# Kernel tuning notes

Measured on AMD Instinct MI355X. Metric: run time of the kernel, lower is better.

The kernel has to match this reference:

```python
import jax, jax.numpy as jnp
import numpy as np

N_NODES = 50000
N_EDGES = 800000
HID = 64
N_LAYERS = 3
N_GRAPHS = 64
NEG_SLOPE = 0.01  # nn.LeakyReLU default


def setup_inputs() -> dict:
    key = jax.random.key(0)
    ks = jax.random.split(key, 10)
    return {
        "x": jax.random.normal(ks[0], (N_NODES, HID), dtype=jnp.float32),
        "edge_attr": jax.random.normal(ks[1], (N_EDGES,), dtype=jnp.float32),
        "edge_w": jax.random.normal(ks[2], (N_LAYERS, 1, HID), dtype=jnp.float32) * 0.1,
        "edge_b": jax.random.normal(ks[3], (N_LAYERS, HID), dtype=jnp.float32) * 0.1,
        "node_w": jax.random.normal(ks[4], (N_LAYERS, 2 * HID, HID), dtype=jnp.float32) * 0.05,
        "node_b": jax.random.normal(ks[5], (N_LAYERS, HID), dtype=jnp.float32) * 0.1,
        "fc_w": jax.random.normal(ks[6], (HID, 1), dtype=jnp.float32) * 0.1,
        "fc_b": jax.random.normal(ks[7], (1,), dtype=jnp.float32) * 0.1,
        "edge_index": jax.random.randint(ks[8], (2, N_EDGES), 0, N_NODES, dtype=jnp.int32),
        "batch": jnp.sort(jax.random.randint(ks[9], (N_NODES,), 0, N_GRAPHS, dtype=jnp.int32)),
    }


def reference(x, edge_attr, edge_w, edge_b, node_w, node_b, fc_w, fc_b, edge_index, batch):
    src = edge_index[0]  # x_j gathered from source nodes
    dst = edge_index[1]  # aggregated into target nodes (aggr='add')
    ea = edge_attr.reshape(-1, 1)  # [E, 1]
    for l in range(N_LAYERS):
        edge_emb = ea @ edge_w[l] + edge_b[l]                       # [E, H] edge MLP
        msg = jnp.concatenate([x[src], edge_emb], axis=1)            # [E, 2H] message
        aggr = jax.ops.segment_sum(msg, dst, num_segments=N_NODES)   # [N, 2H] scatter-add
        x = jax.nn.relu(aggr @ node_w[l] + node_b[l])                # update: node MLP + ReLU
        x = jnp.where(x >= 0, x, NEG_SLOPE * x)                      # LeakyReLU (dropout=0)
    # global_mean_pool over batch assignment
    sums = jax.ops.segment_sum(x, batch, num_segments=N_GRAPHS)      # [G, H]
    counts = jax.ops.segment_sum(jnp.ones((x.shape[0], 1), x.dtype), batch, num_segments=N_GRAPHS)
    pooled = sums / jnp.maximum(counts, 1.0)
    return pooled @ fc_w + fc_b  # [G, 1]
```

## Files before the change

### kernel.cpp

```cpp
#include <hip/hip_runtime.h>

#define N_NODES 50000
#define N_EDGES 800000
#define HID 64
#define N_LAYERS 3
#define N_GRAPHS 64
#define MAXDEG 64
#define FIXS 4096.0f
#define NBUCK 196
#define CAP 8064
#define SCB 4096

typedef unsigned int u32;
typedef unsigned short ushort_t;
typedef short bf16x8 __attribute__((ext_vector_type(8)));
typedef float f32x4 __attribute__((ext_vector_type(4)));
typedef float f32x2 __attribute__((ext_vector_type(2)));

__device__ __forceinline__ ushort_t f2bf(float f) {
    unsigned int u = __builtin_bit_cast(unsigned int, f);
    unsigned int r = u + 0x7fffu + ((u >> 16) & 1u);
    return (ushort_t)(r >> 16);
}
__device__ __forceinline__ unsigned char f2fp8(float f) {
    u32 p = __builtin_amdgcn_cvt_pk_fp8_f32(f, f, 0u, false);
    return (unsigned char)(p & 0xFFu);
}

__global__ __launch_bounds__(256) void cvt_gb_uv_kernel(
        const float* __restrict__ x_in, uint2* __restrict__ xf8,
        const int* __restrict__ batch, int* __restrict__ gstart,
        int* __restrict__ bucketCur,
        const float* __restrict__ edge_w, const float* __restrict__ edge_b,
        const float* __restrict__ node_w, float* __restrict__ uv,
        const float* __restrict__ fc_b, float* __restrict__ out,
        int cvtBlocks, int gbBlocks) {
    int t = threadIdx.x;
    int b = (int)blockIdx.x;
    if (b < cvtBlocks) {
        int i = b * 256 + t;
        if (i < N_NODES * HID / 8) {
            const float4* p = (const float4*)(x_in + (size_t)i * 8);
            float4 a = p[0], c = p[1];
            u32 lo = __builtin_amdgcn_cvt_pk_fp8_f32(a.x, a.y, 0u, false);
            lo      = __builtin_amdgcn_cvt_pk_fp8_f32(a.z, a.w, lo, true);
            u32 hi = __builtin_amdgcn_cvt_pk_fp8_f32(c.x, c.y, 0u, false);
            hi      = __builtin_amdgcn_cvt_pk_fp8_f32(c.z, c.w, hi, true);
            uint2 o; o.x = lo; o.y = hi;
            xf8[i] = o;
        }
        return;
    }
    if (b < cvtBlocks + gbBlocks) {
        int i = (b - cvtBlocks) * 256 + t;
        if (i >= N_NODES) return;
        if (i < NBUCK) bucketCur[i] = i * CAP;
        int bi = batch[i];
        if (i == 0) {
            for (int g = 0; g <= bi; g++) gstart[g] = 0;
        } else {
            int bp = batch[i - 1];
            for (int g = bp + 1; g <= bi; g++) gstart[g] = i;
        }
        if (i == N_NODES - 1) {
            for (int g = bi + 1; g <= N_GRAPHS; g++) gstart[g] = N_NODES;
        }
        return;
    }
    if (t >= 192) {
        if (t < 192 + N_GRAPHS) out[t - 192] = fc_b[0];
        return;
    }
    int l = t >> 6, hp = t & 63;
    const float* w2 = node_w + l * 2 * HID * HID + HID * HID + hp;
    float u = 0.f, v = 0.f;
    for (int h = 0; h < HID; h++) {
        float w = w2[h * HID];
        u += edge_w[l * HID + h] * w;
        v += edge_b[l * HID + h] * w;
    }
    uv[l * 2 * HID + hp]       = u;
    uv[l * 2 * HID + HID + hp] = v;
}

__global__ __launch_bounds__(256) void scatter_kernel(
        const int* __restrict__ src, const int* __restrict__ dst,
        const float* __restrict__ ea, int* __restrict__ bucketCur,
        uint2* __restrict__ recs) {
    __shared__ u32 hist[256], pfx[256], excl[256], baseL[256], limL[256];
    __shared__ uint2 stage[SCB];
    int t = threadIdx.x;
    int b0 = blockIdx.x * SCB;
    int nE = N_EDGES - b0; if (nE > SCB) nE = SCB;
    hist[t] = 0;
    __syncthreads();
    for (int i = t; i < nE; i += 256)
        atomicAdd(&hist[(dst[b0 + i] >> 8) & 255], 1u);
    __syncthreads();
    pfx[t] = hist[t];
    __syncthreads();
    for (int off = 1; off < 256; off <<= 1) {
        u32 v = (t >= off) ? pfx[t - off] : 0u;
        __syncthreads();
        pfx[t] += v;
        __syncthreads();
    }
    u32 cntv = hist[t];
    u32 ex = pfx[t] - cntv;
    excl[t] = ex;
    u32 gbase = (u32)t * CAP;
    if (cntv > 0 && t < NBUCK) {
        gbase = (u32)atomicAdd(&bucketCur[t], (int)cntv);
        u32 lim = (u32)(t + 1) * CAP;
        if (gbase + cntv > lim) cntv = (gbase < lim) ? (lim - gbase) : 0u;
    }
    baseL[t] = gbase;
    limL[t]  = ex + cntv;
    hist[t]  = ex;
    __syncthreads();
    for (int i = t; i < nE; i += 256) {
        int e = b0 + i;
        int d = dst[e];
        int s = src[e];
        float fv = (ea[e] + 8.0f) * FIXS;
        fv = fminf(fmaxf(fv, 0.0f), 65535.0f);
        u32 fx = __float2uint_rn(fv);
        u32 idx = atomicAdd(&hist[(d >> 8) & 255], 1u);
        uint2 r; r.x = (u32)s | (fx << 16); r.y = (u32)d;
        if (idx < (u32)SCB) stage[idx] = r;
    }
    __syncthreads();
    for (int i = t; i < nE; i += 256) {
        uint2 r = stage[i];
        u32 bk = (r.y >> 8) & 255;
        if (bk < NBUCK && (u32)i < limL[bk])
            recs[(size_t)baseL[bk] + ((u32)i - excl[bk])] = r;
    }
}

__global__ __launch_bounds__(256) void build_ell_kernel(
        const uint2* __restrict__ recs, const int* __restrict__ bucketCur,
        u32* __restrict__ ell, int* __restrict__ cnt) {
    __shared__ u32 hist[256], pfx[256], excl[256];
    __shared__ u32 stagePay[CAP];
    __shared__ ushort_t nodeOf[CAP];
    int t = threadIdx.x;
    int b = blockIdx.x;
    size_t eBase = (size_t)b * CAP;
    int m = bucketCur[b] - b * CAP;
    if (m > CAP) m = CAP;
    if (m < 0) m = 0;
    hist[t] = 0;
    __syncthreads();
    for (int i = t; i < m; i += 256)
        atomicAdd(&hist[recs[eBase + i].y & 255], 1u);
    __syncthreads();
    pfx[t] = hist[t];
    __syncthreads();
    for (int off = 1; off < 256; off <<= 1) {
        u32 v = (t >= off) ? pfx[t - off] : 0u;
        __syncthreads();
        pfx[t] += v;
        __syncthreads();
    }
    u32 full = hist[t];
    u32 ex = pfx[t] - full;
    excl[t] = ex;
    u32 cv = full > MAXDEG ? MAXDEG : full;
    int node = b * 256 + t;
    if (node < N_NODES) cnt[node] = (int)cv;
    for (u32 r = 0; r < full && (ex + r) < (u32)CAP; r++) nodeOf[ex + r] = (ushort_t)t;
    hist[t] = ex;
    __syncthreads();
    for (int i = t; i < m; i += 256) {
        uint2 r = recs[eBase + i];
        u32 idx = atomicAdd(&hist[r.y & 255], 1u);
        if (idx < (u32)CAP) stagePay[idx] = r.x;
    }
    __syncthreads();
    for (int i = t; i < m; i += 256) {
        u32 n8 = nodeOf[i];
        u32 rank = (u32)i - excl[n8];
        if (rank < MAXDEG)
            ell[((size_t)(b * 256 + n8) << 6) + rank] = stagePay[i];
    }
}

__global__ __launch_bounds__(256) void agg_mfma_kernel(
        const unsigned char* __restrict__ xf8, const u32* __restrict__ ell,
        const int* __restrict__ cnt,
        const float* __restrict__ W1, const float* __restrict__ node_b_l,
        const float* __restrict__ uv_l, float* __restrict__ sattr,
        int layer0, unsigned char* __restrict__ out_f8, float* __restrict__ out_f32) {
    __shared__ float red[4][64][9];
    __shared__ u32   redS[4][8];
    int lane = threadIdx.x & 63;
    int w = threadIdx.x >> 6;
    int nodeBase = blockIdx.x * 16;
    int oct = lane & 7, n8 = lane >> 3;
    int pairSel = w >> 1;
    int kslice = w & 1;

    int m = nodeBase + pairSel * 8 + n8;
    int dg = cnt[m]; if (dg > MAXDEG) dg = MAXDEG;
    int mx = dg;
#pragma unroll
    for (int off = 8; off < 64; off <<= 1) {
        int o = __shfl_xor(mx, off);
        mx = o > mx ? o : mx;
    }

    const uint4* erow4 = (const uint4*)(ell + ((size_t)m << 6));
    const uint2* xrows = (const uint2*)xf8;
    float accC[8] = {0,0,0,0,0,0,0,0};
    u32 sfix = 0;
    int base = kslice * 4;
    uint4 e4 = {0, 0, 0, 0};
    if (base < mx) e4 = erow4[base >> 2];
    for (; base < mx; base += 8) {
        int nbase = base + 8;
        uint4 e4n = {0, 0, 0, 0};
        if (nbase < mx) e4n = erow4[nbase >> 2];
        u32 ee[4] = {e4.x, e4.y, e4.z, e4.w};
        uint2 rw[4];
        float f[4];
#pragma unroll
        for (int k = 0; k < 4; k++) {
            bool v = (base + k) < dg;
            sfix += (v && oct == 0) ? (ee[k] >> 16) : 0u;
            int s = v ? (int)(ee[k] & 0xffffu) : 0;
            rw[k] = xrows[(size_t)s * 8 + oct];
            f[k] = v ? 1.0f : 0.0f;
        }
#pragma unroll
        for (int k = 0; k < 4; k++) {
            f32x2 p0 = __builtin_amdgcn_cvt_pk_f32_fp8(rw[k].x, false);
            f32x2 p1 = __builtin_amdgcn_cvt_pk_f32_fp8(rw[k].x, true);
            f32x2 p2 = __builtin_amdgcn_cvt_pk_f32_fp8(rw[k].y, false);
            f32x2 p3 = __builtin_amdgcn_cvt_pk_f32_fp8(rw[k].y, true);
            accC[0] += f[k] * p0[0]; accC[1] += f[k] * p0[1];
            accC[2] += f[k] * p1[0]; accC[3] += f[k] * p1[1];
            accC[4] += f[k] * p2[0]; accC[5] += f[k] * p2[1];
            accC[6] += f[k] * p3[0]; accC[7] += f[k] * p3[1];
        }
        e4 = e4n;
    }

#pragma unroll
    for (int j = 0; j < 8; j++) red[w][lane][j] = accC[j];
    if (oct == 0) redS[w][n8] = sfix;
    __syncthreads();
    if (w != 0) return;

    int q = lane >> 4, n15 = lane & 15;
    int w0 = (n15 >> 3) * 2;
    int h8 = (n15 & 7) * 8;
    float accA[8], accB[8];
#pragma unroll
    for (int j = 0; j < 8; j++) {
        accA[j] = red[w0][h8 + q][j]     + red[w0 + 1][h8 + q][j];
        accB[j] = red[w0][h8 + 4 + q][j] + red[w0 + 1][h8 + 4 + q][j];
    }
    u32 sfix2 = redS[w0][n15 & 7] + redS[w0 + 1][n15 & 7];
    int m2 = nodeBase + n15;
    int dg2 = cnt[m2]; if (dg2 > MAXDEG) dg2 = MAXDEG;

    float satv;
    if (layer0) {
        satv = (float)(int)sfix2 * (1.0f / FIXS) - 8.0f * (float)dg2;
        if (lane < 16) sattr[m2] = satv;
    } else {
        satv = sattr[m2];
    }

    bf16x8 af0, af1;
#pragma unroll
    for (int j = 0; j < 8; j++) {
        af0[j] = (short)f2bf(accA[j]);
        af1[j] = (short)f2bf(accB[j]);
    }

    int q8 = q * 8;
    f32x4 c[4];
#pragma unroll
    for (int nt = 0; nt < 4; nt++) {
        bf16x8 b0, b1;
#pragma unroll
        for (int j = 0; j < 8; j++) {
            b0[j] = (short)f2bf(W1[(q8 + j) * HID + nt * 16 + n15]);
            b1[j] = (short)f2bf(W1[(32 + q8 + j) * HID + nt * 16 + n15]);
        }
        f32x4 z = {0.f, 0.f, 0.f, 0.f};
        c[nt] = __builtin_amdgcn_mfma_f32_16x16x32_bf16(af0, b0, z, 0, 0, 0);
        c[nt] = __builtin_amdgcn_mfma_f32_16x16x32_bf16(af1, b1, c[nt], 0, 0, 0);
    }

    float dgown = (float)dg2;
    float sat[4], dgf[4];
#pragma unroll
    for (int r = 0; r < 4; r++) {
        int srcLane = q * 4 + r;
        sat[r] = __shfl(satv, srcLane);
        dgf[r] = __shfl(dgown, srcLane);
    }
#pragma unroll
    for (int nt = 0; nt < 4; nt++) {
        int col = nt * 16 + n15;
        float uc = uv_l[col], vc = uv_l[HID + col], bc = node_b_l[col];
#pragma unroll
        for (int r = 0; r < 4; r++) {
            int n = nodeBase + q * 4 + r;
            float val = c[nt][r] + sat[r] * uc + dgf[r] * vc + bc;
            val = val > 0.f ? val : 0.f;
            if (out_f8) out_f8[(size_t)n * HID + col] = f2fp8(val);
            else        out_f32[(size_t)n * HID + col] = val;
        }
    }
}

__global__ __launch_bounds__(256) void pool_fc_kernel(
        const float* __restrict__ x, const int* __restrict__ gstart,
        const float* __restrict__ fc_w, float* __restrict__ out) {
    __shared__ float red[4][HID];
    int g = blockIdx.x >> 3, s8 = blockIdx.x & 7;
    int lane = threadIdx.x & 63, w = threadIdx.x >> 6;
    int s = gstart[g], e = gstart[g + 1];
    float acc = 0.f;
    int r = s + s8 * 4 + w;
    for (; r + 96 < e; r += 128) {
        float a0 = x[(size_t)(r     ) * HID + lane];
        float a1 = x[(size_t)(r + 32) * HID + lane];
        float a2 = x[(size_t)(r + 64) * HID + lane];
        float a3 = x[(size_t)(r + 96) * HID + lane];
        acc += a0 + a1 + a2 + a3;
    }
    for (; r < e; r += 32) acc += x[(size_t)r * HID + lane];
    red[w][lane] = acc;
    __syncthreads();
    if (w != 0) return;
    acc = red[0][lane] + red[1][lane] + red[2][lane] + red[3][lane];
    float dot = acc * fc_w[lane];
    for (int off = 32; off > 0; off >>= 1) dot += __shfl_down(dot, off);
    if (lane == 0) {
        float cntf = (float)(e - s);
        if (cntf < 1.f) cntf = 1.f;
        atomicAdd(&out[g], dot / cntf);
    }
}

extern "C" void kernel_launch(void* const* d_in, const int* in_sizes, int n_in,
                              void* d_out, int out_size, void* d_ws, size_t ws_size,
                              hipStream_t stream) {
    const float* x_in      = (const float*)d_in[0];
    const float* edge_attr = (const float*)d_in[1];
    const float* edge_w    = (const float*)d_in[2];
    const float* edge_b    = (const float*)d_in[3];
    const float* node_w    = (const float*)d_in[4];
    const float* node_b    = (const float*)d_in[5];
    const float* fc_w      = (const float*)d_in[6];
    const float* fc_b      = (const float*)d_in[7];
    const int*   edge_index= (const int*)d_in[8];
    const int*   batch     = (const int*)d_in[9];
    float* out = (float*)d_out;

    unsigned char* xf8_0 = (unsigned char*)d_ws;
    unsigned char* xf8_1 = xf8_0 + (size_t)N_NODES * HID;
    float*    xA    = (float*)(xf8_1 + (size_t)N_NODES * HID);
    uint2*    recs  = (uint2*)xA;
    u32*      ell   = (u32*)(xA + (size_t)N_NODES * HID);
    int*      cnt   = (int*)(ell + (size_t)N_NODES * MAXDEG);
    int*      gstart= cnt + N_NODES;
    float*    sattr = (float*)(gstart + N_GRAPHS + 1);
    float*    uv    = sattr + N_NODES;
    int*      bucketCur = (int*)(uv + N_LAYERS * 2 * HID);

    const int* src = edge_index;
    const int* dst = edge_index + N_EDGES;

    const int CVT = (N_NODES * HID / 8 + 255) / 256;
    const int GB  = (N_NODES + 255) / 256;
    cvt_gb_uv_kernel<<<CVT + GB + 1, 256, 0, stream>>>(
        x_in, (uint2*)xf8_0, batch, gstart, bucketCur,
        edge_w, edge_b, node_w, uv, fc_b, out, CVT, GB);

    scatter_kernel<<<(N_EDGES + SCB - 1) / SCB, 256, 0, stream>>>(
        src, dst, edge_attr, bucketCur, recs);
    build_ell_kernel<<<NBUCK, 256, 0, stream>>>(recs, bucketCur, ell, cnt);

    const int AGG_BLOCKS = N_NODES / 16;
    agg_mfma_kernel<<<AGG_BLOCKS, 256, 0, stream>>>(
        xf8_0, ell, cnt, node_w, node_b, uv, sattr, 1, xf8_1, nullptr);
    agg_mfma_kernel<<<AGG_BLOCKS, 256, 0, stream>>>(
        xf8_1, ell, cnt, node_w + (size_t)2 * HID * HID, node_b + HID, uv + 2 * HID,
        sattr, 0, xf8_0, nullptr);
    agg_mfma_kernel<<<AGG_BLOCKS, 256, 0, stream>>>(
        xf8_0, ell, cnt, node_w + (size_t)4 * HID * HID, node_b + 2 * HID, uv + 4 * HID,
        sattr, 0, nullptr, xA);

    pool_fc_kernel<<<N_GRAPHS * 8, 256, 0, stream>>>(xA, gstart, fc_w, out);
}
```

Baseline: 179.8 us.

## Fuse scatter into front kernel, split ELL build, widen aggregation gathers

Merges the edge bucket-scatter kernel into the conversion/batch-start kernel and resets the bucket cursors with a memset, which removes one launch. The scatter tile shrinks so more blocks run at once. The ELL build now splits each bucket across four blocks of 64 nodes; each block rescans the whole bucket but needs far less shared memory. The aggregation kernel gathers 16 fp8 bytes per lane with 4 lanes per node and splits the edges four ways across waves, which adds a larger cross-wave reduction.

```diff
diff --git a/kernel.cpp b/kernel.cpp
--- a/kernel.cpp
+++ b/kernel.cpp
@@ -9,7 +9,8 @@
 #define FIXS 4096.0f
 #define NBUCK 196
 #define CAP 8064
-#define SCB 4096
+#define CAP2 1600
+#define SCB 2048
 
 typedef unsigned int u32;
 typedef unsigned short ushort_t;
@@ -27,18 +28,71 @@
     return (unsigned char)(p & 0xFFu);
 }
 
-__global__ __launch_bounds__(256) void cvt_gb_uv_kernel(
+__global__ __launch_bounds__(256) void fused_front_kernel(
+        const int* __restrict__ src, const int* __restrict__ dst,
+        const float* __restrict__ ea, int* __restrict__ bucketCur,
+        uint2* __restrict__ recs,
         const float* __restrict__ x_in, uint2* __restrict__ xf8,
         const int* __restrict__ batch, int* __restrict__ gstart,
-        int* __restrict__ bucketCur,
         const float* __restrict__ edge_w, const float* __restrict__ edge_b,
         const float* __restrict__ node_w, float* __restrict__ uv,
         const float* __restrict__ fc_b, float* __restrict__ out,
-        int cvtBlocks, int gbBlocks) {
+        int scBlocks, int cvtBlocks, int gbBlocks) {
+    __shared__ u32 hist[256], pfx[256], excl[256], baseL[256], limL[256];
+    __shared__ uint2 stage[SCB];
     int t = threadIdx.x;
     int b = (int)blockIdx.x;
-    if (b < cvtBlocks) {
-        int i = b * 256 + t;
+    if (b < scBlocks) {
+        int b0 = b * SCB;
+        int nE = N_EDGES - b0; if (nE > SCB) nE = SCB;
+        hist[t] = 0;
+        __syncthreads();
+        for (int i = t; i < nE; i += 256)
+            atomicAdd(&hist[(dst[b0 + i] >> 8) & 255], 1u);
+        __syncthreads();
+        pfx[t] = hist[t];
+        __syncthreads();
+        for (int off = 1; off < 256; off <<= 1) {
+            u32 v = (t >= off) ? pfx[t - off] : 0u;
+            __syncthreads();
+            pfx[t] += v;
+            __syncthreads();
+        }
+        u32 cntv = hist[t];
+        u32 ex = pfx[t] - cntv;
+        excl[t] = ex;
+        u32 gbase = 0;
+        if (cntv > 0 && t < NBUCK) {
+            u32 start = (u32)atomicAdd(&bucketCur[t], (int)cntv);
+            if (start + cntv > (u32)CAP) cntv = (start < (u32)CAP) ? (u32)CAP - start : 0u;
+            gbase = (u32)t * CAP + start;
+        }
+        baseL[t] = gbase;
+        limL[t]  = ex + cntv;
+        hist[t]  = ex;
+        __syncthreads();
+        for (int i = t; i < nE; i += 256) {
+            int e = b0 + i;
+            int d = dst[e];
+            int s = src[e];
+            float fv = (ea[e] + 8.0f) * FIXS;
+            fv = fminf(fmaxf(fv, 0.0f), 65535.0f);
+            u32 fx = __float2uint_rn(fv);
+            u32 idx = atomicAdd(&hist[(d >> 8) & 255], 1u);
+            uint2 r; r.x = (u32)s | (fx << 16); r.y = (u32)d;
+            if (idx < (u32)SCB) stage[idx] = r;
+        }
+        __syncthreads();
+        for (int i = t; i < nE; i += 256) {
+            uint2 r = stage[i];
+            u32 bk = (r.y >> 8) & 255;
+            if (bk < NBUCK && (u32)i < limL[bk])
+                recs[(size_t)baseL[bk] + ((u32)i - excl[bk])] = r;
+        }
+        return;
+    }
+    if (b < scBlocks + cvtBlocks) {
+        int i = (b - scBlocks) * 256 + t;
         if (i < N_NODES * HID / 8) {
             const float4* p = (const float4*)(x_in + (size_t)i * 8);
             float4 a = p[0], c = p[1];
@@ -51,10 +105,9 @@
         }
         return;
     }
-    if (b < cvtBlocks + gbBlocks) {
-        int i = (b - cvtBlocks) * 256 + t;
+    if (b < scBlocks + cvtBlocks + gbBlocks) {
+        int i = (b - scBlocks - cvtBlocks) * 256 + t;
         if (i >= N_NODES) return;
-        if (i < NBUCK) bucketCur[i] = i * CAP;
         int bi = batch[i];
         if (i == 0) {
             for (int g = 0; g <= bi; g++) gstart[g] = 0;
@@ -83,106 +136,58 @@
     uv[l * 2 * HID + HID + hp] = v;
 }
 
-__global__ __launch_bounds__(256) void scatter_kernel(
-        const int* __restrict__ src, const int* __restrict__ dst,
-        const float* __restrict__ ea, int* __restrict__ bucketCur,
-        uint2* __restrict__ recs) {
-    __shared__ u32 hist[256], pfx[256], excl[256], baseL[256], limL[256];
-    __shared__ uint2 stage[SCB];
-    int t = threadIdx.x;
-    int b0 = blockIdx.x * SCB;
-    int nE = N_EDGES - b0; if (nE > SCB) nE = SCB;
-    hist[t] = 0;
-    __syncthreads();
-    for (int i = t; i < nE; i += 256)
-        atomicAdd(&hist[(dst[b0 + i] >> 8) & 255], 1u);
-    __syncthreads();
-    pfx[t] = hist[t];
-    __syncthreads();
-    for (int off = 1; off < 256; off <<= 1) {
-        u32 v = (t >= off) ? pfx[t - off] : 0u;
-        __syncthreads();
-        pfx[t] += v;
-        __syncthreads();
-    }
-    u32 cntv = hist[t];
-    u32 ex = pfx[t] - cntv;
-    excl[t] = ex;
-    u32 gbase = (u32)t * CAP;
-    if (cntv > 0 && t < NBUCK) {
-        gbase = (u32)atomicAdd(&bucketCur[t], (int)cntv);
-        u32 lim = (u32)(t + 1) * CAP;
-        if (gbase + cntv > lim) cntv = (gbase < lim) ? (lim - gbase) : 0u;
-    }
-    baseL[t] = gbase;
-    limL[t]  = ex + cntv;
-    hist[t]  = ex;
-    __syncthreads();
-    for (int i = t; i < nE; i += 256) {
-        int e = b0 + i;
-        int d = dst[e];
-        int s = src[e];
-        float fv = (ea[e] + 8.0f) * FIXS;
-        fv = fminf(fmaxf(fv, 0.0f), 65535.0f);
-        u32 fx = __float2uint_rn(fv);
-        u32 idx = atomicAdd(&hist[(d >> 8) & 255], 1u);
-        uint2 r; r.x = (u32)s | (fx << 16); r.y = (u32)d;
-        if (idx < (u32)SCB) stage[idx] = r;
-    }
-    __syncthreads();
-    for (int i = t; i < nE; i += 256) {
-        uint2 r = stage[i];
-        u32 bk = (r.y >> 8) & 255;
-        if (bk < NBUCK && (u32)i < limL[bk])
-            recs[(size_t)baseL[bk] + ((u32)i - excl[bk])] = r;
-    }
-}
-
 __global__ __launch_bounds__(256) void build_ell_kernel(
         const uint2* __restrict__ recs, const int* __restrict__ bucketCur,
         u32* __restrict__ ell, int* __restrict__ cnt) {
-    __shared__ u32 hist[256], pfx[256], excl[256];
-    __shared__ u32 stagePay[CAP];
-    __shared__ ushort_t nodeOf[CAP];
+    __shared__ u32 hist[64], pfx[64], excl[64];
+    __shared__ u32 stagePay[CAP2];
+    __shared__ ushort_t nodeOf[CAP2];
     int t = threadIdx.x;
-    int b = blockIdx.x;
+    int b = blockIdx.x >> 2, sub = blockIdx.x & 3;
     size_t eBase = (size_t)b * CAP;
-    int m = bucketCur[b] - b * CAP;
+    int m = bucketCur[b];
     if (m > CAP) m = CAP;
     if (m < 0) m = 0;
-    hist[t] = 0;
-    __syncthreads();
-    for (int i = t; i < m; i += 256)
-        atomicAdd(&hist[recs[eBase + i].y & 255], 1u);
-    __syncthreads();
-    pfx[t] = hist[t];
-    __syncthreads();
-    for (int off = 1; off < 256; off <<= 1) {
-        u32 v = (t >= off) ? pfx[t - off] : 0u;
-        __syncthreads();
-        pfx[t] += v;
-        __syncthreads();
-    }
-    u32 full = hist[t];
-    u32 ex = pfx[t] - full;
-    excl[t] = ex;
-    u32 cv = full > MAXDEG ? MAXDEG : full;
-    int node = b * 256 + t;
-    if (node < N_NODES) cnt[node] = (int)cv;
-    for (u32 r = 0; r < full && (ex + r) < (u32)CAP; r++) nodeOf[ex + r] = (ushort_t)t;
-    hist[t] = ex;
-    __syncthreads();
+    if (t < 64) hist[t] = 0;
+    __syncthreads();
+    for (int i = t; i < m; i += 256) {
+        u32 y = recs[eBase + i].y;
+        if ((int)((y >> 6) & 3) == sub) atomicAdd(&hist[y & 63], 1u);
+    }
+    __syncthreads();
+    if (t < 64) pfx[t] = hist[t];
+    __syncthreads();
+    for (int off = 1; off < 64; off <<= 1) {
+        u32 v = (t < 64 && t >= off) ? pfx[t - off] : 0u;
+        __syncthreads();
+        if (t < 64) pfx[t] += v;
+        __syncthreads();
+    }
+    int node = b * 256 + sub * 64 + (t & 63);
+    if (t < 64) {
+        u32 full = hist[t];
+        u32 ex = pfx[t] - full;
+        excl[t] = ex;
+        if (node < N_NODES) cnt[node] = (int)(full > MAXDEG ? MAXDEG : full);
+        for (u32 r = 0; r < full && (ex + r) < (u32)CAP2; r++) nodeOf[ex + r] = (ushort_t)t;
+        hist[t] = ex;
+    }
+    __syncthreads();
+    int tot = (int)pfx[63];
+    if (tot > CAP2) tot = CAP2;
     for (int i = t; i < m; i += 256) {
         uint2 r = recs[eBase + i];
-        u32 idx = atomicAdd(&hist[r.y & 255], 1u);
-        if (idx < (u32)CAP) stagePay[idx] = r.x;
-    }
-    __syncthreads();
-    for (int i = t; i < m; i += 256) {
-        u32 n8 = nodeOf[i];
-        u32 rank = (u32)i - excl[n8];
+        if ((int)((r.y >> 6) & 3) == sub) {
+            u32 idx = atomicAdd(&hist[r.y & 63], 1u);
+            if (idx < (u32)CAP2) stagePay[idx] = r.x;
+        }
+    }
+    __syncthreads();
+    for (int i = t; i < tot; i += 256) {
+        u32 n64 = nodeOf[i];
+        u32 rank = (u32)i - excl[n64];
         if (rank < MAXDEG)
-            ell[((size_t)(b * 256 + n8) << 6) + rank] = stagePay[i];
+            ell[((size_t)(b * 256 + sub * 64 + n64) << 6) + rank] = stagePay[i];
     }
 }
 
@@ -192,76 +197,80 @@
         const float* __restrict__ W1, const float* __restrict__ node_b_l,
         const float* __restrict__ uv_l, float* __restrict__ sattr,
         int layer0, unsigned char* __restrict__ out_f8, float* __restrict__ out_f32) {
-    __shared__ float red[4][64][9];
-    __shared__ u32   redS[4][8];
+    __shared__ float red[4][64][17];
+    __shared__ u32   redS[4][16];
     int lane = threadIdx.x & 63;
     int w = threadIdx.x >> 6;
     int nodeBase = blockIdx.x * 16;
-    int oct = lane & 7, n8 = lane >> 3;
-    int pairSel = w >> 1;
-    int kslice = w & 1;
-
-    int m = nodeBase + pairSel * 8 + n8;
+    int n16 = lane >> 2, q4 = lane & 3;
+
+    int m = nodeBase + n16;
     int dg = cnt[m]; if (dg > MAXDEG) dg = MAXDEG;
     int mx = dg;
 #pragma unroll
-    for (int off = 8; off < 64; off <<= 1) {
+    for (int off = 4; off < 64; off <<= 1) {
         int o = __shfl_xor(mx, off);
         mx = o > mx ? o : mx;
     }
 
     const uint4* erow4 = (const uint4*)(ell + ((size_t)m << 6));
-    const uint2* xrows = (const uint2*)xf8;
-    float accC[8] = {0,0,0,0,0,0,0,0};
+    const uint4* xq = (const uint4*)xf8;
+    float acc[16];
+#pragma unroll
+    for (int j = 0; j < 16; j++) acc[j] = 0.f;
     u32 sfix = 0;
-    int base = kslice * 4;
+    int base = w * 4;
     uint4 e4 = {0, 0, 0, 0};
     if (base < mx) e4 = erow4[base >> 2];
-    for (; base < mx; base += 8) {
-        int nbase = base + 8;
+    for (; base < mx; base += 16) {
+        int nbase = base + 16;
         uint4 e4n = {0, 0, 0, 0};
         if (nbase < mx) e4n = erow4[nbase >> 2];
         u32 ee[4] = {e4.x, e4.y, e4.z, e4.w};
-        uint2 rw[4];
+        uint4 rw[4];
         float f[4];
 #pragma unroll
         for (int k = 0; k < 4; k++) {
             bool v = (base + k) < dg;
-            sfix += (v && oct == 0) ? (ee[k] >> 16) : 0u;
+            sfix += (v && q4 == 0) ? (ee[k] >> 16) : 0u;
             int s = v ? (int)(ee[k] & 0xffffu) : 0;
-            rw[k] = xrows[(size_t)s * 8 + oct];
+            rw[k] = xq[(size_t)s * 4 + q4];
             f[k] = v ? 1.0f : 0.0f;
         }
 #pragma unroll
         for (int k = 0; k < 4; k++) {
-            f32x2 p0 = __builtin_amdgcn_cvt_pk_f32_fp8(rw[k].x, false);
-            f32x2 p1 = __builtin_amdgcn_cvt_pk_f32_fp8(rw[k].x, true);
-            f32x2 p2 = __builtin_amdgcn_cvt_pk_f32_fp8(rw[k].y, false);
-            f32x2 p3 = __builtin_amdgcn_cvt_pk_f32_fp8(rw[k].y, true);
-            accC[0] += f[k] * p0[0]; accC[1] += f[k] * p0[1];
-            accC[2] += f[k] * p1[0]; accC[3] += f[k] * p1[1];
-            accC[4] += f[k] * p2[0]; accC[5] += f[k] * p2[1];
-            accC[6] += f[k] * p3[0]; accC[7] += f[k] * p3[1];
+            u32 dw[4] = {rw[k].x, rw[k].y, rw[k].z, rw[k].w};
+#pragma unroll
+            for (int d0 = 0; d0 < 4; d0++) {
+                f32x2 plo = __builtin_amdgcn_cvt_pk_f32_fp8(dw[d0], false);
+                f32x2 phi = __builtin_amdgcn_cvt_pk_f32_fp8(dw[d0], true);
+                acc[d0 * 4 + 0] += f[k] * plo[0];
+                acc[d0 * 4 + 1] += f[k] * plo[1];
+                acc[d0 * 4 + 2] += f[k] * phi[0];
+                acc[d0 * 4 + 3] += f[k] * phi[1];
+            }
         }
         e4 = e4n;
     }
 
 #pragma unroll
-    for (int j = 0; j < 8; j++) red[w][lane][j] = accC[j];
-    if (oct == 0) redS[w][n8] = sfix;
+    for (int j = 0; j < 16; j++) red[w][lane][j] = acc[j];
+    if (q4 == 0) redS[w][n16] = sfix;
     __syncthreads();
     if (w != 0) return;
 
     int q = lane >> 4, n15 = lane & 15;
-    int w0 = (n15 >> 3) * 2;
-    int h8 = (n15 & 7) * 8;
     float accA[8], accB[8];
 #pragma unroll
     for (int j = 0; j < 8; j++) {
-        accA[j] = red[w0][h8 + q][j]     + red[w0 + 1][h8 + q][j];
-        accB[j] = red[w0][h8 + 4 + q][j] + red[w0 + 1][h8 + 4 + q][j];
-    }
-    u32 sfix2 = redS[w0][n15 & 7] + redS[w0 + 1][n15 & 7];
+        int fA = 8 * q + j;
+        int fB = 32 + 8 * q + j;
+        int lA = n15 * 4 + (fA >> 4), eA = fA & 15;
+        int lB = n15 * 4 + (fB >> 4), eB = fB & 15;
+        accA[j] = red[0][lA][eA] + red[1][lA][eA] + red[2][lA][eA] + red[3][lA][eA];
+        accB[j] = red[0][lB][eB] + red[1][lB][eB] + red[2][lB][eB] + red[3][lB][eB];
+    }
+    u32 sfix2 = redS[0][n15] + redS[1][n15] + redS[2][n15] + redS[3][n15];
     int m2 = nodeBase + n15;
     int dg2 = cnt[m2]; if (dg2 > MAXDEG) dg2 = MAXDEG;
 
@@ -377,15 +386,17 @@
     const int* src = edge_index;
     const int* dst = edge_index + N_EDGES;
 
+    hipMemsetAsync(bucketCur, 0, NBUCK * sizeof(int), stream);
+
+    const int SC  = (N_EDGES + SCB - 1) / SCB;
     const int CVT = (N_NODES * HID / 8 + 255) / 256;
     const int GB  = (N_NODES + 255) / 256;
-    cvt_gb_uv_kernel<<<CVT + GB + 1, 256, 0, stream>>>(
-        x_in, (uint2*)xf8_0, batch, gstart, bucketCur,
-        edge_w, edge_b, node_w, uv, fc_b, out, CVT, GB);
-
-    scatter_kernel<<<(N_EDGES + SCB - 1) / SCB, 256, 0, stream>>>(
-        src, dst, edge_attr, bucketCur, recs);
-    build_ell_kernel<<<NBUCK, 256, 0, stream>>>(recs, bucketCur, ell, cnt);
+    fused_front_kernel<<<SC + CVT + GB + 1, 256, 0, stream>>>(
+        src, dst, edge_attr, bucketCur, recs,
+        x_in, (uint2*)xf8_0, batch, gstart,
+        edge_w, edge_b, node_w, uv, fc_b, out, SC, CVT, GB);
+
+    build_ell_kernel<<<NBUCK * 4, 256, 0, stream>>>(recs, bucketCur, ell, cnt);
 
     const int AGG_BLOCKS = N_NODES / 16;
     agg_mfma_kernel<<<AGG_BLOCKS, 256, 0, stream>>>(
```

Measured after the change: 179.2 us (median of 2 runs). About the same (-0.3%).
